# Performance work log

Hardware: AMD Instinct MI355X
Metric: run time of the kernel (lower is better)

## Reference

```python
import jax, jax.numpy as jnp
import numpy as np

B, C, H, W = 2, 512, 64, 64
NH = 8
EPS = 1e-5


def setup_inputs() -> dict:
    key = jax.random.key(0)
    ks = jax.random.split(key, 4)
    s_in = 1.0 / np.sqrt(C)
    x = jax.random.normal(ks[0], (B, C, H, W), dtype=jnp.float32)
    qkv_w = jax.random.normal(ks[1], (3 * C, C), dtype=jnp.float32) * s_in
    qkv_b = jnp.zeros((3 * C,), dtype=jnp.float32)
    out_w = jax.random.normal(ks[2], (C, C), dtype=jnp.float32) * s_in
    out_b = jnp.zeros((C,), dtype=jnp.float32)
    ln_g = jnp.ones((C,), dtype=jnp.float32)
    ln_b = jnp.zeros((C,), dtype=jnp.float32)
    return {"x": x, "qkv_w": qkv_w, "qkv_b": qkv_b, "out_w": out_w,
            "out_b": out_b, "ln_g": ln_g, "ln_b": ln_b, "num_heads": NH}


def reference(x, qkv_w, qkv_b, out_w, out_b, ln_g, ln_b, num_heads):
    b, c, h, w = x.shape
    n = h * w
    hd = c // num_heads
    scale = hd ** -0.5

    # flatten spatial: [B, N, C]
    tokens = x.reshape(b, c, n).transpose(0, 2, 1)

    # fused QKV projection
    qkv = tokens @ qkv_w.T + qkv_b            # [B, N, 3C]
    q, k, v = jnp.split(qkv, 3, axis=-1)

    def heads(t):  # [B, N, C] -> [B, H, N, D]
        return t.reshape(b, n, num_heads, hd).transpose(0, 2, 1, 3)

    q, k, v = heads(q), heads(k), heads(v)

    # naive full attention (materializes [B, H, N, N] as in the original)
    scores = jnp.einsum('bhqd,bhkd->bhqk', q, k) * scale
    attn = jax.nn.softmax(scores, axis=-1)
    out = jnp.einsum('bhqk,bhkd->bhqd', attn, v)  # [B, H, N, D]

    out = out.transpose(0, 2, 1, 3).reshape(b, n, c)
    attended = out @ out_w.T + out_b          # [B, N, C]

    # residual + LayerNorm over channels
    res = attended + tokens
    mean = jnp.mean(res, axis=-1, keepdims=True)
    var = jnp.var(res, axis=-1, keepdims=True)
    y = (res - mean) * jax.lax.rsqrt(var + EPS) * ln_g + ln_b

    return y.transpose(0, 2, 1).reshape(b, c, h, w)
```

## Files before the change

kernel.cpp:

```cpp
#include <hip/hip_runtime.h>

#define BATCH 2
#define CH    512
#define NTOK  4096
#define NH    8
#define HD    64
#define MTOT  (BATCH*NTOK)

typedef __attribute__((ext_vector_type(8))) __bf16 bf16x8;
typedef __attribute__((ext_vector_type(4))) float  f32x4;
typedef __attribute__((ext_vector_type(4))) unsigned short u16x4;

static __device__ __forceinline__ f32x4 mfma16(bf16x8 a, bf16x8 b, f32x4 c) {
  return __builtin_amdgcn_mfma_f32_16x16x32_bf16(a, b, c, 0, 0, 0);
}

static __device__ __forceinline__ unsigned short f2bf(float f) {
  unsigned int u = __float_as_uint(f);
  u += 0x7fffu + ((u >> 16) & 1u);
  return (unsigned short)(u >> 16);
}

static __device__ __forceinline__ void gload_lds16(const unsigned short* g, unsigned short* l) {
  __builtin_amdgcn_global_load_lds((const __attribute__((address_space(1))) void*)g,
                                   (__attribute__((address_space(3))) void*)l, 16, 0, 0);
}

#define QSC 0.18033688011112042f

__global__ __launch_bounds__(256) void k_pre(const float* __restrict__ x,
                                             const float* __restrict__ w1,
                                             const float* __restrict__ w2,
                                             unsigned short* __restrict__ tokB,
                                             unsigned short* __restrict__ o1,
                                             unsigned short* __restrict__ o2) {
  __shared__ float tile[32][33];
  int bid = blockIdx.x;
  if (bid >= 4096) {
    int i = (bid - 4096) * 256 + threadIdx.x;
    if (i < 3 * CH * CH) o1[i] = f2bf(w1[i]);
    else o2[i - 3 * CH * CH] = f2bf(w2[i - 3 * CH * CH]);
    return;
  }
  int b  = bid >> 11;
  int n0 = (bid & 127) * 32;
  int c0 = ((bid >> 7) & 15) * 32;
  int tx = threadIdx.x & 31, ty = threadIdx.x >> 5;
#pragma unroll
  for (int i = 0; i < 4; i++) {
    int c = c0 + ty + 8 * i;
    tile[ty + 8 * i][tx] = x[((size_t)b * CH + c) * NTOK + n0 + tx];
  }
  __syncthreads();
#pragma unroll
  for (int i = 0; i < 4; i++) {
    int n = n0 + ty + 8 * i;
    int c = c0 + tx;
    tokB[((size_t)b * NTOK + n) * CH + c] = f2bf(tile[tx][ty + 8 * i]);
  }
}

#define BK 64

static __device__ __forceinline__ void stage_g(const unsigned short* __restrict__ src,
                                               size_t row0, int k0,
                                               unsigned short* __restrict__ lds,
                                               int wid, int lane) {
  int sub = lane >> 3;
  int ch  = (lane & 7) ^ sub;
#pragma unroll
  for (int i = 0; i < 4; i++) {
    int rbase = 32 * wid + 8 * i;
    gload_lds16(&src[(row0 + rbase + sub) * 512 + k0 + ch * 8], &lds[rbase * BK]);
  }
}

static __device__ __forceinline__ void stage_g64(const unsigned short* __restrict__ src,
                                                 size_t row0, int k0,
                                                 unsigned short* __restrict__ lds,
                                                 int wid, int lane) {
  int sub = lane >> 3;
  int ch  = (lane & 7) ^ sub;
#pragma unroll
  for (int i = 0; i < 2; i++) {
    int rbase = 16 * wid + 8 * i;
    gload_lds16(&src[(row0 + rbase + sub) * 512 + k0 + ch * 8], &lds[rbase * BK]);
  }
}

static __device__ __forceinline__ bf16x8 frag_ld(const unsigned short* __restrict__ lds,
                                                 int row, int ks, int lane) {
  int ch = ((ks << 2) + (lane >> 4)) ^ (row & 7);
  return *reinterpret_cast<const bf16x8*>(&lds[row * BK + ch * 8]);
}

__global__ __launch_bounds__(256) void k_gemm_qkv(const unsigned short* __restrict__ A,
                                                  const unsigned short* __restrict__ W,
                                                  const float* __restrict__ bias,
                                                  unsigned short* __restrict__ qb,
                                                  unsigned short* __restrict__ kb,
                                                  unsigned short* __restrict__ vt) {
  __shared__ unsigned short lsA[128 * BK];
  __shared__ unsigned short lsB[128 * BK];
  int bm0 = blockIdx.x * 128;
  int bn0 = blockIdx.y * 128;
  int tid = threadIdx.x, lane = tid & 63, wid = tid >> 6;
  int wm = wid >> 1, wn = wid & 1;

  f32x4 acc[4][4];
  f32x4 zz = {0.f, 0.f, 0.f, 0.f};
#pragma unroll
  for (int i = 0; i < 4; i++)
#pragma unroll
    for (int j = 0; j < 4; j++) acc[i][j] = zz;

  for (int k0 = 0; k0 < 512; k0 += BK) {
    stage_g(A, (size_t)bm0, k0, lsA, wid, lane);
    stage_g(W, (size_t)bn0, k0, lsB, wid, lane);
    __syncthreads();
#pragma unroll
    for (int ks = 0; ks < 2; ks++) {
      bf16x8 af[4], bfr[4];
#pragma unroll
      for (int t = 0; t < 4; t++) {
        af[t]  = frag_ld(lsA, wm * 64 + t * 16 + (lane & 15), ks, lane);
        bfr[t] = frag_ld(lsB, wn * 64 + t * 16 + (lane & 15), ks, lane);
      }
#pragma unroll
      for (int mt = 0; mt < 4; mt++)
#pragma unroll
        for (int nt = 0; nt < 4; nt++) acc[mt][nt] = mfma16(af[mt], bfr[nt], acc[mt][nt]);
    }
    __syncthreads();
  }
#pragma unroll
  for (int nt = 0; nt < 4; nt++) {
    int j = bn0 + wn * 64 + nt * 16 + (lane & 15);
    float bj = bias[j];
    int which = j >> 9;
    int cp = j & 511;
    int h = cp >> 6, d = cp & 63;
    if (which == 2) {
#pragma unroll
      for (int mt = 0; mt < 4; mt++) {
        int m = bm0 + wm * 64 + mt * 16 + 4 * (lane >> 4);
        int b = m >> 12, n = m & 4095;
        u16x4 pk;
#pragma unroll
        for (int r = 0; r < 4; r++) pk[r] = f2bf(acc[mt][nt][r] + bj);
        *reinterpret_cast<u16x4*>(&vt[((size_t)((b * NH + h) * HD + d)) * NTOK + n]) = pk;
      }
    } else {
      unsigned short* dst = (which == 0) ? qb : kb;
      float sc = (which == 0) ? QSC : 1.0f;
#pragma unroll
      for (int mt = 0; mt < 4; mt++) {
#pragma unroll
        for (int r = 0; r < 4; r++) {
          int m = bm0 + wm * 64 + mt * 16 + 4 * (lane >> 4) + r;
          int b = m >> 12, n = m & 4095;
          dst[(((size_t)(b * NH + h) * NTOK + n) << 6) + d] = f2bf((acc[mt][nt][r] + bj) * sc);
        }
      }
    }
  }
}

#define KVB 64
#define NT  (NTOK / KVB)

static __device__ __forceinline__ void stage_kv(const unsigned short* __restrict__ Kp,
                                                const unsigned short* __restrict__ Vp,
                                                unsigned short* __restrict__ lk,
                                                unsigned short* __restrict__ lv,
                                                int kv0, int wid, int lane) {
  int sub = lane >> 3;
  int c7  = lane & 7;
#pragma unroll
  for (int i = 0; i < 2; i++) {
    int rbase = 16 * wid + 8 * i;
    int row = rbase + sub;
    int fk = (sub & 3) | (i << 2);
    gload_lds16(&Kp[((size_t)(kv0 + row) << 6) + ((c7 ^ fk) << 3)], &lk[rbase << 6]);
    gload_lds16(&Vp[(size_t)row * NTOK + kv0 + ((c7 ^ sub) << 3)], &lv[rbase << 6]);
  }
}

static __device__ __forceinline__ void attn_tile(const unsigned short* __restrict__ lk,
                                                 const unsigned short* __restrict__ lv,
                                                 int half,
                                                 const bf16x8 qf[2][2],
                                                 f32x4* oacc0, f32x4* oacc1,
                                                 f32x4& lacc0, f32x4& lacc1,
                                                 bf16x8 onesf, int g, int lr) {
  f32x4 zz = {0.f, 0.f, 0.f, 0.f};
  int l7 = lr & 7;
  int tbase = 32 * half + 8 * (lr >> 2) + (lr & 3);
  int kc0 = (g ^ l7) << 3;
  int kc1 = ((4 + g) ^ l7) << 3;
  bf16x8 kf[2][2];
#pragma unroll
  for (int ct = 0; ct < 2; ct++) {
    int t = tbase + 4 * ct;
    kf[ct][0] = *reinterpret_cast<const bf16x8*>(&lk[(t << 6) + kc0]);
    kf[ct][1] = *reinterpret_cast<const bf16x8*>(&lk[(t << 6) + kc1]);
  }
  f32x4 s0[2], s1[2];
#pragma unroll
  for (int ct = 0; ct < 2; ct++) {
    s0[ct] = mfma16(kf[ct][0], qf[0][0], zz);
    s0[ct] = mfma16(kf[ct][1], qf[0][1], s0[ct]);
    s1[ct] = mfma16(kf[ct][0], qf[1][0], zz);
    s1[ct] = mfma16(kf[ct][1], qf[1][1], s1[ct]);
  }
  bf16x8 vf[4];
  int vc = (((half << 2) + g) ^ l7) << 3;
#pragma unroll
  for (int dt = 0; dt < 4; dt++)
    vf[dt] = *reinterpret_cast<const bf16x8*>(&lv[((dt * 16 + lr) << 6) + vc]);
#pragma unroll
  for (int ct = 0; ct < 2; ct++) {
#pragma unroll
    for (int r = 0; r < 4; r++) {
      s0[ct][r] = __builtin_exp2f(s0[ct][r]);
      s1[ct][r] = __builtin_exp2f(s1[ct][r]);
    }
  }
  unsigned int w0[2][2], w1[2][2];
#pragma unroll
  for (int ct = 0; ct < 2; ct++) {
    asm("v_cvt_pk_bf16_f32 %0, %1, %2" : "=v"(w0[ct][0]) : "v"(s0[ct][0]), "v"(s0[ct][1]));
    asm("v_cvt_pk_bf16_f32 %0, %1, %2" : "=v"(w0[ct][1]) : "v"(s0[ct][2]), "v"(s0[ct][3]));
    asm("v_cvt_pk_bf16_f32 %0, %1, %2" : "=v"(w1[ct][0]) : "v"(s1[ct][0]), "v"(s1[ct][1]));
    asm("v_cvt_pk_bf16_f32 %0, %1, %2" : "=v"(w1[ct][1]) : "v"(s1[ct][2]), "v"(s1[ct][3]));
  }
  union U { unsigned int w[4]; bf16x8 v; };
  U a0, b0;
  a0.w[0] = w0[0][0]; a0.w[1] = w0[0][1]; a0.w[2] = w0[1][0]; a0.w[3] = w0[1][1];
  b0.w[0] = w1[0][0]; b0.w[1] = w1[0][1]; b0.w[2] = w1[1][0]; b0.w[3] = w1[1][1];
#pragma unroll
  for (int dt = 0; dt < 4; dt++) {
    oacc0[dt] = mfma16(a0.v, vf[dt], oacc0[dt]);
    oacc1[dt] = mfma16(b0.v, vf[dt], oacc1[dt]);
  }
  lacc0 = mfma16(a0.v, onesf, lacc0);
  lacc1 = mfma16(b0.v, onesf, lacc1);
}

__global__ __launch_bounds__(256, 4) void k_attn(const unsigned short* __restrict__ Q,
                                                 const unsigned short* __restrict__ K,
                                                 const unsigned short* __restrict__ Vt,
                                                 unsigned short* __restrict__ O) {
  __shared__ unsigned short lsK[2][KVB * 64];
  __shared__ unsigned short lsV[2][64 * KVB];
  int gid = blockIdx.x;
  int vv  = (gid & 7) * 128 + (gid >> 3);
  int bh  = vv >> 6;
  int tid = threadIdx.x, lane = tid & 63, wid = tid >> 6;
  int pair = wid >> 1, half = wid & 1;
  int g = lane >> 4, lr = lane & 15;
  int qw = (vv & 63) * 64 + pair * 32;
  const unsigned short* Qp = Q + (size_t)bh * NTOK * HD;
  const unsigned short* Kp = K + (size_t)bh * NTOK * HD;
  const unsigned short* Vp = Vt + (size_t)bh * HD * NTOK;
  unsigned short* K0 = &lsK[0][0]; unsigned short* K1 = &lsK[1][0];
  unsigned short* V0 = &lsV[0][0]; unsigned short* V1 = &lsV[1][0];

  union { unsigned short u[8]; bf16x8 v; } ou;
#pragma unroll
  for (int i = 0; i < 8; i++) ou.u[i] = 0x3F80;
  bf16x8 onesf = ou.v;

  bf16x8 qf[2][2];
#pragma unroll
  for (int sq = 0; sq < 2; sq++)
#pragma unroll
    for (int ks = 0; ks < 2; ks++)
      qf[sq][ks] = *reinterpret_cast<const bf16x8*>(
          &Qp[(size_t)(qw + sq * 16 + lr) * HD + ks * 32 + 8 * g]);

  f32x4 zz = {0.f, 0.f, 0.f, 0.f};
  f32x4 oacc0[4] = {zz, zz, zz, zz};
  f32x4 oacc1[4] = {zz, zz, zz, zz};
  f32x4 lacc0 = zz, lacc1 = zz;

  stage_kv(Kp, Vp, K0, V0, 0, wid, lane);
  __syncthreads();

  for (int t = 0; t < NT; t += 2) {
    stage_kv(Kp, Vp, K1, V1, (t + 1) * KVB, wid, lane);
    attn_tile(K0, V0, half, qf, oacc0, oacc1, lacc0, lacc1, onesf, g, lr);
    __syncthreads();
    if (t + 2 < NT) stage_kv(Kp, Vp, K0, V0, (t + 2) * KVB, wid, lane);
    attn_tile(K1, V1, half, qf, oacc0, oacc1, lacc0, lacc1, onesf, g, lr);
    __syncthreads();
  }
  float* mO = (float*)&lsK[0][0];
  float* mL = (float*)&lsV[0][0];
  if (half) {
#pragma unroll
    for (int sq = 0; sq < 2; sq++) {
      f32x4* oacc = sq ? oacc1 : oacc0;
      f32x4  lacc = sq ? lacc1 : lacc0;
#pragma unroll
      for (int r = 0; r < 4; r++) {
        int q = pair * 32 + sq * 16 + 4 * g + r;
#pragma unroll
        for (int dt = 0; dt < 4; dt++) mO[(q << 6) + dt * 16 + lr] = oacc[dt][r];
        if (lr == 0) mL[q] = lacc[r];
      }
    }
  }
  __syncthreads();
  if (!half) {
    int b2 = bh >> 3, h = bh & 7;
#pragma unroll
    for (int sq = 0; sq < 2; sq++) {
      f32x4* oacc = sq ? oacc1 : oacc0;
      f32x4  lacc = sq ? lacc1 : lacc0;
#pragma unroll
      for (int r = 0; r < 4; r++) {
        int q = pair * 32 + sq * 16 + 4 * g + r;
        float inv = 1.0f / (lacc[r] + mL[q]);
        int n = qw + sq * 16 + 4 * g + r;
#pragma unroll
        for (int dt = 0; dt < 4; dt++) {
          int d = dt * 16 + lr;
          float o = oacc[dt][r] + mO[(q << 6) + dt * 16 + lr];
          O[((size_t)(b2 * NTOK + n)) * CH + h * HD + d] = f2bf(o * inv);
        }
      }
    }
  }
}

__global__ __launch_bounds__(256) void k_gemm_out(const unsigned short* __restrict__ A,
                                                  const unsigned short* __restrict__ W,
                                                  const float* __restrict__ bias,
                                                  const unsigned short* __restrict__ tokB,
                                                  unsigned short* __restrict__ res) {
  __shared__ unsigned short lsA[64 * BK];
  __shared__ unsigned short lsB[128 * BK];
  int bm0 = blockIdx.x * 64;
  int bn0 = blockIdx.y * 128;
  int tid = threadIdx.x, lane = tid & 63, wid = tid >> 6;
  int wm = wid >> 1, wn = wid & 1;

  f32x4 acc[2][4];
  f32x4 zz = {0.f, 0.f, 0.f, 0.f};
#pragma unroll
  for (int i = 0; i < 2; i++)
#pragma unroll
    for (int j = 0; j < 4; j++) acc[i][j] = zz;

  for (int k0 = 0; k0 < 512; k0 += BK) {
    stage_g64(A, (size_t)bm0, k0, lsA, wid, lane);
    stage_g(W, (size_t)bn0, k0, lsB, wid, lane);
    __syncthreads();
#pragma unroll
    for (int ks = 0; ks < 2; ks++) {
      bf16x8 af[2], bfr[4];
#pragma unroll
      for (int t = 0; t < 2; t++)
        af[t] = frag_ld(lsA, wm * 32 + t * 16 + (lane & 15), ks, lane);
#pragma unroll
      for (int t = 0; t < 4; t++)
        bfr[t] = frag_ld(lsB, wn * 64 + t * 16 + (lane & 15), ks, lane);
#pragma unroll
      for (int mt = 0; mt < 2; mt++)
#pragma unroll
        for (int nt = 0; nt < 4; nt++) acc[mt][nt] = mfma16(af[mt], bfr[nt], acc[mt][nt]);
    }
    __syncthreads();
  }
#pragma unroll
  for (int nt = 0; nt < 4; nt++) {
    int j = bn0 + wn * 64 + nt * 16 + (lane & 15);
    float bj = bias[j];
#pragma unroll
    for (int mt = 0; mt < 2; mt++) {
#pragma unroll
      for (int r = 0; r < 4; r++) {
        int m = bm0 + wm * 32 + mt * 16 + 4 * (lane >> 4) + r;
        size_t idx = (size_t)m * CH + j;
        float tk = __uint_as_float((unsigned int)tokB[idx] << 16);
        res[idx] = f2bf(acc[mt][nt][r] + bj + tk);
      }
    }
  }
}

__global__ __launch_bounds__(256) void k_ln(const unsigned short* __restrict__ res,
                                            const float* __restrict__ g,
                                            const float* __restrict__ bb,
                                            float* __restrict__ y) {
  __shared__ float smean[32], srstd[32];
  int m0 = blockIdx.x * 32;
  int tid = threadIdx.x, lane = tid & 63, wid = tid >> 6;
  for (int t = 0; t < 8; t++) {
    int idx = wid * 8 + t;
    uint4 v = *reinterpret_cast<const uint4*>(&res[(size_t)(m0 + idx) * CH + lane * 8]);
    unsigned int wv[4] = {v.x, v.y, v.z, v.w};
    float s = 0.f, ss = 0.f;
#pragma unroll
    for (int j = 0; j < 4; j++) {
      float lo = __uint_as_float(wv[j] << 16);
      float hi = __uint_as_float(wv[j] & 0xFFFF0000u);
      s += lo + hi; ss += lo * lo + hi * hi;
    }
#pragma unroll
    for (int off = 1; off < 64; off <<= 1) {
      s += __shfl_xor(s, off);
      ss += __shfl_xor(ss, off);
    }
    if (lane == 0) {
      float mean = s * (1.0f / CH);
      float var = ss * (1.0f / CH) - mean * mean;
      smean[idx] = mean;
      srstd[idx] = rsqrtf(var + 1e-5f);
    }
  }
  __syncthreads();
  int b = m0 >> 12, n0 = m0 & 4095;
  int tn = tid & 31;
  int cq = tid >> 5;
  float mn = smean[tn], rs = srstd[tn];
  const unsigned short* rrow = res + (size_t)(m0 + tn) * CH;
  float* yb = y + ((size_t)b * CH) * NTOK + n0 + tn;
#pragma unroll
  for (int i = 0; i < 8; i++) {
    int c = cq * 64 + i * 8;
    uint4 v = *reinterpret_cast<const uint4*>(&rrow[c]);
    unsigned int wv[4] = {v.x, v.y, v.z, v.w};
    float4 ga = *reinterpret_cast<const float4*>(&g[c]);
    float4 gb = *reinterpret_cast<const float4*>(&g[c + 4]);
    float4 ba = *reinterpret_cast<const float4*>(&bb[c]);
    float4 b4 = *reinterpret_cast<const float4*>(&bb[c + 4]);
    float gg[8] = {ga.x, ga.y, ga.z, ga.w, gb.x, gb.y, gb.z, gb.w};
    float bv[8] = {ba.x, ba.y, ba.z, ba.w, b4.x, b4.y, b4.z, b4.w};
#pragma unroll
    for (int j = 0; j < 4; j++) {
      float lo = __uint_as_float(wv[j] << 16);
      float hi = __uint_as_float(wv[j] & 0xFFFF0000u);
      yb[(size_t)(c + 2 * j) * NTOK]     = (lo - mn) * rs * gg[2 * j]     + bv[2 * j];
      yb[(size_t)(c + 2 * j + 1) * NTOK] = (hi - mn) * rs * gg[2 * j + 1] + bv[2 * j + 1];
    }
  }
}

extern "C" void kernel_launch(void* const* d_in, const int* in_sizes, int n_in,
                              void* d_out, int out_size, void* d_ws, size_t ws_size,
                              hipStream_t stream) {
  const float* x    = (const float*)d_in[0];
  const float* qkvw = (const float*)d_in[1];
  const float* qkvb = (const float*)d_in[2];
  const float* outw = (const float*)d_in[3];
  const float* outb = (const float*)d_in[4];
  const float* lng  = (const float*)d_in[5];
  const float* lnb  = (const float*)d_in[6];
  float* y = (float*)d_out;

  const size_t NC = (size_t)MTOT * CH;
  char* ws = (char*)d_ws;
  size_t off = 0;
  auto nxt = [&](size_t bytes) -> void* {
    void* p = ws + off;
    off += (bytes + 255) & ~(size_t)255;
    return p;
  };
  unsigned short* tokB = (unsigned short*)nxt(NC * 2);
  unsigned short* wqkv = (unsigned short*)nxt((size_t)3 * CH * CH * 2);
  unsigned short* wout = (unsigned short*)nxt((size_t)CH * CH * 2);
  unsigned short* qb   = (unsigned short*)nxt(NC * 2);
  unsigned short* kb   = (unsigned short*)nxt(NC * 2);
  unsigned short* vt   = (unsigned short*)nxt(NC * 2);
  unsigned short* ao   = (unsigned short*)nxt(NC * 2);
  unsigned short* resb = (unsigned short*)nxt(NC * 2);
  if (off > ws_size) return;

  k_pre<<<8192, 256, 0, stream>>>(x, qkvw, outw, tokB, wqkv, wout);
  k_gemm_qkv<<<dim3(MTOT / 128, (3 * CH) / 128), 256, 0, stream>>>(tokB, wqkv, qkvb, qb, kb, vt);
  k_attn<<<1024, 256, 0, stream>>>(qb, kb, vt, ao);
  k_gemm_out<<<dim3(MTOT / 64, CH / 128), 256, 0, stream>>>(ao, wout, outb, tokB, resb);
  k_ln<<<MTOT / 32, 256, 0, stream>>>(resb, lng, lnb, y);
}
```

Baseline: 157.6 us.

## Load K/V fragments directly from global memory instead of LDS double-buffering

The attention kernel drops the shared-memory double-buffered K/V staging and its per-tile barriers. Each wave now reads its K and transposed-V fragments straight from global memory into registers inside the KV loop, relying on L1/L2 for reuse across waves. This removes LDS traffic and __syncthreads stalls, but every wave now issues its own global loads, so data shared across the block's waves is fetched redundantly and may be less coalesced.

```diff
diff --git a/kernel.cpp b/kernel.cpp
--- a/kernel.cpp
+++ b/kernel.cpp
@@ -169,90 +169,12 @@
 #define KVB 64
 #define NT  (NTOK / KVB)
 
-static __device__ __forceinline__ void stage_kv(const unsigned short* __restrict__ Kp,
-                                                const unsigned short* __restrict__ Vp,
-                                                unsigned short* __restrict__ lk,
-                                                unsigned short* __restrict__ lv,
-                                                int kv0, int wid, int lane) {
-  int sub = lane >> 3;
-  int c7  = lane & 7;
-#pragma unroll
-  for (int i = 0; i < 2; i++) {
-    int rbase = 16 * wid + 8 * i;
-    int row = rbase + sub;
-    int fk = (sub & 3) | (i << 2);
-    gload_lds16(&Kp[((size_t)(kv0 + row) << 6) + ((c7 ^ fk) << 3)], &lk[rbase << 6]);
-    gload_lds16(&Vp[(size_t)row * NTOK + kv0 + ((c7 ^ sub) << 3)], &lv[rbase << 6]);
-  }
-}
-
-static __device__ __forceinline__ void attn_tile(const unsigned short* __restrict__ lk,
-                                                 const unsigned short* __restrict__ lv,
-                                                 int half,
-                                                 const bf16x8 qf[2][2],
-                                                 f32x4* oacc0, f32x4* oacc1,
-                                                 f32x4& lacc0, f32x4& lacc1,
-                                                 bf16x8 onesf, int g, int lr) {
-  f32x4 zz = {0.f, 0.f, 0.f, 0.f};
-  int l7 = lr & 7;
-  int tbase = 32 * half + 8 * (lr >> 2) + (lr & 3);
-  int kc0 = (g ^ l7) << 3;
-  int kc1 = ((4 + g) ^ l7) << 3;
-  bf16x8 kf[2][2];
-#pragma unroll
-  for (int ct = 0; ct < 2; ct++) {
-    int t = tbase + 4 * ct;
-    kf[ct][0] = *reinterpret_cast<const bf16x8*>(&lk[(t << 6) + kc0]);
-    kf[ct][1] = *reinterpret_cast<const bf16x8*>(&lk[(t << 6) + kc1]);
-  }
-  f32x4 s0[2], s1[2];
-#pragma unroll
-  for (int ct = 0; ct < 2; ct++) {
-    s0[ct] = mfma16(kf[ct][0], qf[0][0], zz);
-    s0[ct] = mfma16(kf[ct][1], qf[0][1], s0[ct]);
-    s1[ct] = mfma16(kf[ct][0], qf[1][0], zz);
-    s1[ct] = mfma16(kf[ct][1], qf[1][1], s1[ct]);
-  }
-  bf16x8 vf[4];
-  int vc = (((half << 2) + g) ^ l7) << 3;
-#pragma unroll
-  for (int dt = 0; dt < 4; dt++)
-    vf[dt] = *reinterpret_cast<const bf16x8*>(&lv[((dt * 16 + lr) << 6) + vc]);
-#pragma unroll
-  for (int ct = 0; ct < 2; ct++) {
-#pragma unroll
-    for (int r = 0; r < 4; r++) {
-      s0[ct][r] = __builtin_exp2f(s0[ct][r]);
-      s1[ct][r] = __builtin_exp2f(s1[ct][r]);
-    }
-  }
-  unsigned int w0[2][2], w1[2][2];
-#pragma unroll
-  for (int ct = 0; ct < 2; ct++) {
-    asm("v_cvt_pk_bf16_f32 %0, %1, %2" : "=v"(w0[ct][0]) : "v"(s0[ct][0]), "v"(s0[ct][1]));
-    asm("v_cvt_pk_bf16_f32 %0, %1, %2" : "=v"(w0[ct][1]) : "v"(s0[ct][2]), "v"(s0[ct][3]));
-    asm("v_cvt_pk_bf16_f32 %0, %1, %2" : "=v"(w1[ct][0]) : "v"(s1[ct][0]), "v"(s1[ct][1]));
-    asm("v_cvt_pk_bf16_f32 %0, %1, %2" : "=v"(w1[ct][1]) : "v"(s1[ct][2]), "v"(s1[ct][3]));
-  }
-  union U { unsigned int w[4]; bf16x8 v; };
-  U a0, b0;
-  a0.w[0] = w0[0][0]; a0.w[1] = w0[0][1]; a0.w[2] = w0[1][0]; a0.w[3] = w0[1][1];
-  b0.w[0] = w1[0][0]; b0.w[1] = w1[0][1]; b0.w[2] = w1[1][0]; b0.w[3] = w1[1][1];
-#pragma unroll
-  for (int dt = 0; dt < 4; dt++) {
-    oacc0[dt] = mfma16(a0.v, vf[dt], oacc0[dt]);
-    oacc1[dt] = mfma16(b0.v, vf[dt], oacc1[dt]);
-  }
-  lacc0 = mfma16(a0.v, onesf, lacc0);
-  lacc1 = mfma16(b0.v, onesf, lacc1);
-}
-
 __global__ __launch_bounds__(256, 4) void k_attn(const unsigned short* __restrict__ Q,
                                                  const unsigned short* __restrict__ K,
                                                  const unsigned short* __restrict__ Vt,
                                                  unsigned short* __restrict__ O) {
-  __shared__ unsigned short lsK[2][KVB * 64];
-  __shared__ unsigned short lsV[2][64 * KVB];
+  __shared__ float mO[2][32][64];
+  __shared__ float mL[2][32];
   int gid = blockIdx.x;
   int vv  = (gid & 7) * 128 + (gid >> 3);
   int bh  = vv >> 6;
@@ -261,10 +183,8 @@
   int g = lane >> 4, lr = lane & 15;
   int qw = (vv & 63) * 64 + pair * 32;
   const unsigned short* Qp = Q + (size_t)bh * NTOK * HD;
-  const unsigned short* Kp = K + (size_t)bh * NTOK * HD;
-  const unsigned short* Vp = Vt + (size_t)bh * HD * NTOK;
-  unsigned short* K0 = &lsK[0][0]; unsigned short* K1 = &lsK[1][0];
-  unsigned short* V0 = &lsV[0][0]; unsigned short* V1 = &lsV[1][0];
+  const unsigned short* Kp = K + ((size_t)bh * NTOK + 32 * half) * HD;
+  const unsigned short* Vp = Vt + (size_t)bh * HD * NTOK + 32 * half;
 
   union { unsigned short u[8]; bf16x8 v; } ou;
 #pragma unroll
@@ -284,19 +204,61 @@
   f32x4 oacc1[4] = {zz, zz, zz, zz};
   f32x4 lacc0 = zz, lacc1 = zz;
 
-  stage_kv(Kp, Vp, K0, V0, 0, wid, lane);
-  __syncthreads();
-
-  for (int t = 0; t < NT; t += 2) {
-    stage_kv(Kp, Vp, K1, V1, (t + 1) * KVB, wid, lane);
-    attn_tile(K0, V0, half, qf, oacc0, oacc1, lacc0, lacc1, onesf, g, lr);
-    __syncthreads();
-    if (t + 2 < NT) stage_kv(Kp, Vp, K0, V0, (t + 2) * KVB, wid, lane);
-    attn_tile(K1, V1, half, qf, oacc0, oacc1, lacc0, lacc1, onesf, g, lr);
-    __syncthreads();
-  }
-  float* mO = (float*)&lsK[0][0];
-  float* mL = (float*)&lsV[0][0];
+  int tbase = 8 * (lr >> 2) + (lr & 3);
+  const unsigned short* Kl = Kp + (size_t)tbase * HD + 8 * g;
+  const unsigned short* Vl = Vp + 8 * g;
+
+#pragma unroll 2
+  for (int t = 0; t < NT; t++) {
+    const unsigned short* Kt = Kl + (size_t)t * KVB * HD;
+    const unsigned short* Vtp = Vl + t * KVB;
+    bf16x8 kf[2][2];
+#pragma unroll
+    for (int ct = 0; ct < 2; ct++) {
+#pragma unroll
+      for (int ks = 0; ks < 2; ks++)
+        kf[ct][ks] = *reinterpret_cast<const bf16x8*>(&Kt[(size_t)(4 * ct) * HD + ks * 32]);
+    }
+    f32x4 s0[2], s1[2];
+#pragma unroll
+    for (int ct = 0; ct < 2; ct++) {
+      s0[ct] = mfma16(kf[ct][0], qf[0][0], zz);
+      s0[ct] = mfma16(kf[ct][1], qf[0][1], s0[ct]);
+      s1[ct] = mfma16(kf[ct][0], qf[1][0], zz);
+      s1[ct] = mfma16(kf[ct][1], qf[1][1], s1[ct]);
+    }
+    bf16x8 vf[4];
+#pragma unroll
+    for (int dt = 0; dt < 4; dt++)
+      vf[dt] = *reinterpret_cast<const bf16x8*>(&Vtp[(size_t)(dt * 16 + lr) * NTOK]);
+#pragma unroll
+    for (int ct = 0; ct < 2; ct++) {
+#pragma unroll
+      for (int r = 0; r < 4; r++) {
+        s0[ct][r] = __builtin_exp2f(s0[ct][r]);
+        s1[ct][r] = __builtin_exp2f(s1[ct][r]);
+      }
+    }
+    unsigned int w0[2][2], w1[2][2];
+#pragma unroll
+    for (int ct = 0; ct < 2; ct++) {
+      asm("v_cvt_pk_bf16_f32 %0, %1, %2" : "=v"(w0[ct][0]) : "v"(s0[ct][0]), "v"(s0[ct][1]));
+      asm("v_cvt_pk_bf16_f32 %0, %1, %2" : "=v"(w0[ct][1]) : "v"(s0[ct][2]), "v"(s0[ct][3]));
+      asm("v_cvt_pk_bf16_f32 %0, %1, %2" : "=v"(w1[ct][0]) : "v"(s1[ct][0]), "v"(s1[ct][1]));
+      asm("v_cvt_pk_bf16_f32 %0, %1, %2" : "=v"(w1[ct][1]) : "v"(s1[ct][2]), "v"(s1[ct][3]));
+    }
+    union U { unsigned int w[4]; bf16x8 v; };
+    U a0, b0;
+    a0.w[0] = w0[0][0]; a0.w[1] = w0[0][1]; a0.w[2] = w0[1][0]; a0.w[3] = w0[1][1];
+    b0.w[0] = w1[0][0]; b0.w[1] = w1[0][1]; b0.w[2] = w1[1][0]; b0.w[3] = w1[1][1];
+#pragma unroll
+    for (int dt = 0; dt < 4; dt++) {
+      oacc0[dt] = mfma16(a0.v, vf[dt], oacc0[dt]);
+      oacc1[dt] = mfma16(b0.v, vf[dt], oacc1[dt]);
+    }
+    lacc0 = mfma16(a0.v, onesf, lacc0);
+    lacc1 = mfma16(b0.v, onesf, lacc1);
+  }
   if (half) {
 #pragma unroll
     for (int sq = 0; sq < 2; sq++) {
@@ -304,10 +266,10 @@
       f32x4  lacc = sq ? lacc1 : lacc0;
 #pragma unroll
       for (int r = 0; r < 4; r++) {
-        int q = pair * 32 + sq * 16 + 4 * g + r;
-#pragma unroll
-        for (int dt = 0; dt < 4; dt++) mO[(q << 6) + dt * 16 + lr] = oacc[dt][r];
-        if (lr == 0) mL[q] = lacc[r];
+        int q = sq * 16 + 4 * g + r;
+#pragma unroll
+        for (int dt = 0; dt < 4; dt++) mO[pair][q][dt * 16 + lr] = oacc[dt][r];
+        if (lr == 0) mL[pair][q] = lacc[r];
       }
     }
   }
@@ -320,13 +282,13 @@
       f32x4  lacc = sq ? lacc1 : lacc0;
 #pragma unroll
       for (int r = 0; r < 4; r++) {
-        int q = pair * 32 + sq * 16 + 4 * g + r;
-        float inv = 1.0f / (lacc[r] + mL[q]);
+        int q = sq * 16 + 4 * g + r;
+        float inv = 1.0f / (lacc[r] + mL[pair][q]);
         int n = qw + sq * 16 + 4 * g + r;
 #pragma unroll
         for (int dt = 0; dt < 4; dt++) {
           int d = dt * 16 + lr;
-          float o = oacc[dt][r] + mO[(q << 6) + dt * 16 + lr];
+          float o = oacc[dt][r] + mO[pair][q][dt * 16 + lr];
           O[((size_t)(b2 * NTOK + n)) * CH + h * HD + d] = f2bf(o * inv);
         }
       }
```

Result: slower. 285.5 us (+81.2%).
